# Performance work log

Measured on AMD Instinct MI355X. Metric: run time of the kernel, lower is better.

Reference implementation:

```python
import jax, jax.numpy as jnp
import numpy as np

B, S, D, NH = 4, 2048, 1024, 16
HD = D // NH  # head dim = 64

def setup_inputs() -> dict:
    key = jax.random.key(0)
    ks = jax.random.split(key, 10)
    sc = 0.02
    return {
        "hidden_states": jax.random.normal(ks[0], (B, S, D), jnp.float32),
        "attention_mask": jnp.ones((B, S), jnp.float32),
        "Wq": jax.random.normal(ks[1], (D, D), jnp.float32) * sc,
        "bq": jnp.zeros((D,), jnp.float32),
        "Wk": jax.random.normal(ks[2], (D, D), jnp.float32) * sc,
        "bk": jnp.zeros((D,), jnp.float32),
        "Wv": jax.random.normal(ks[3], (D, D), jnp.float32) * sc,
        "bv": jnp.zeros((D,), jnp.float32),
        "Wo": jax.random.normal(ks[4], (D, D), jnp.float32) * sc,
        "bo": jnp.zeros((D,), jnp.float32),
    }

def reference(hidden_states, attention_mask, Wq, bq, Wk, bk, Wv, bv, Wo, bo):
    # projections: torch Linear computes x @ W.T + b
    q = hidden_states @ Wq.T + bq
    k = hidden_states @ Wk.T + bk
    v = hidden_states @ Wv.T + bv
    # [B,S,D] -> [B,NH,S,HD]
    def split_heads(x):
        return x.reshape(B, S, NH, HD).transpose(0, 2, 1, 3)
    q, k, v = split_heads(q), split_heads(k), split_heads(v)
    scores = jnp.einsum('bhqd,bhkd->bhqk', q, k) / jnp.sqrt(jnp.float32(HD))
    ext_mask = (1.0 - attention_mask)[:, None, None, :] * -10000.0
    scores = scores + ext_mask
    probs = jax.nn.softmax(scores, axis=-1)
    ctx = jnp.einsum('bhqk,bhkd->bhqd', probs, v)
    ctx = ctx.transpose(0, 2, 1, 3).reshape(B, S, D)
    return ctx @ Wo.T + bo
```

## Files before the change

kernel.cpp:

```cpp
#include <hip/hip_runtime.h>

typedef __attribute__((ext_vector_type(8))) short bf16x8;
typedef __attribute__((ext_vector_type(4))) float f32x4;
typedef __attribute__((ext_vector_type(2))) unsigned u32x2;
typedef __attribute__((ext_vector_type(4))) unsigned u32x4;

#define NBATCH 4
#define NSEQ   2048
#define NDIM   1024
#define NHEAD  16
#define HDIM   64

static __device__ __forceinline__ unsigned short f2bf(float f) {
  unsigned u = __float_as_uint(f);
  u += 0x7fffu + ((u >> 16) & 1u);
  return (unsigned short)(u >> 16);
}

static __device__ __forceinline__ unsigned cvt_pk_bf16(float lo, float hi) {
  unsigned d;
  asm("v_cvt_pk_bf16_f32 %0, %1, %2" : "=v"(d) : "v"(lo), "v"(hi));
  return d;
}

static __device__ __forceinline__ void gload16(const void* g, void* l) {
  __builtin_amdgcn_global_load_lds(
      (const __attribute__((address_space(1))) unsigned*)g,
      (__attribute__((address_space(3))) unsigned*)l, 16, 0, 0);
}

__global__ __launch_bounds__(256) void cvt_kernel(
    const float* __restrict__ hs, const float* __restrict__ wq,
    const float* __restrict__ wk, const float* __restrict__ wv,
    const float* __restrict__ wo,
    unsigned short* __restrict__ hsb, unsigned short* __restrict__ wqb,
    unsigned short* __restrict__ wkb, unsigned short* __restrict__ wvb,
    unsigned short* __restrict__ wob) {
  long long t = (long long)blockIdx.x * blockDim.x + threadIdx.x;
  long long i4 = t * 4;
  const float* src; unsigned short* dst; long long base;
  if (i4 < 8388608LL) { src = hs; dst = hsb; base = i4; }
  else {
    long long j = i4 - 8388608LL;
    int w = (int)(j >> 20);
    base = j & 1048575LL;
    switch (w) { case 0: src=wq; dst=wqb; break; case 1: src=wk; dst=wkb; break;
                 case 2: src=wv; dst=wvb; break; default: src=wo; dst=wob; break; }
  }
  float4 v = *(const float4*)(src + base);
  unsigned short r0=f2bf(v.x), r1=f2bf(v.y), r2=f2bf(v.z), r3=f2bf(v.w);
  *(uint2*)(dst + base) = make_uint2((unsigned)r0 | ((unsigned)r1<<16),
                                     (unsigned)r2 | ((unsigned)r3<<16));
}

static __device__ __forceinline__ void gemm128(
    const unsigned short* __restrict__ A, const unsigned short* __restrict__ W,
    unsigned short* As, unsigned short* Bs, int m0, int n0, f32x4 (&acc)[4][4]) {
  const int tid = threadIdx.x;
  const int w = tid >> 6, l = tid & 63, g = l >> 4, r = l & 15;
  const int wm = w >> 1, wn = w & 1;
  const f32x4 z4 = {0.f, 0.f, 0.f, 0.f};
  #pragma unroll
  for (int i = 0; i < 4; ++i)
    #pragma unroll
    for (int j = 0; j < 4; ++j) acc[i][j] = z4;
  const int srow = (l >> 2);
  const int scol = (l & 3) * 8;
  for (int kt = 0; kt < 32; ++kt) {
    const int k0 = kt * 32;
    __syncthreads();
    #pragma unroll
    for (int i = 0; i < 2; ++i) {
      int c8 = w * 2 + i;
      int row = c8 * 16 + srow;
      gload16(A + (size_t)(m0 + row) * 1024 + k0 + scol, As + c8 * 512);
      gload16(W + (size_t)(n0 + row) * 1024 + k0 + scol, Bs + c8 * 512);
    }
    asm volatile("s_waitcnt vmcnt(0)" ::: "memory");
    __syncthreads();
    bf16x8 af[4], bf[4];
    #pragma unroll
    for (int ma = 0; ma < 4; ++ma)
      af[ma] = *(const bf16x8*)(As + (wm*64 + ma*16 + r) * 32 + g * 8);
    #pragma unroll
    for (int nb = 0; nb < 4; ++nb)
      bf[nb] = *(const bf16x8*)(Bs + (wn*64 + nb*16 + r) * 32 + g * 8);
    #pragma unroll
    for (int ma = 0; ma < 4; ++ma)
      #pragma unroll
      for (int nb = 0; nb < 4; ++nb)
        acc[ma][nb] = __builtin_amdgcn_mfma_f32_16x16x32_bf16(
            af[ma], bf[nb], acc[ma][nb], 0, 0, 0);
  }
}

__global__ __launch_bounds__(256) void qkv_gemm(
    const unsigned short* __restrict__ hsb,
    const unsigned short* __restrict__ wqb, const unsigned short* __restrict__ wkb,
    const unsigned short* __restrict__ wvb,
    const float* __restrict__ bq, const float* __restrict__ bk,
    const float* __restrict__ bv,
    unsigned short* __restrict__ qb, unsigned short* __restrict__ kb,
    unsigned short* __restrict__ vtb) {
  __shared__ unsigned short As[128*32], Bs[128*32];
  const int z = blockIdx.z;
  const unsigned short* W = (z == 0) ? wqb : (z == 1) ? wkb : wvb;
  const float* bias = (z == 0) ? bq : (z == 1) ? bk : bv;
  const int m0 = blockIdx.y * 128, n0 = blockIdx.x * 128;
  f32x4 acc[4][4];
  gemm128(hsb, W, As, Bs, m0, n0, acc);
  const int tid = threadIdx.x, w = tid >> 6, l = tid & 63, g = l >> 4, r = l & 15;
  const int wm = w >> 1, wn = w & 1;
  #pragma unroll
  for (int nb = 0; nb < 4; ++nb) {
    int n = n0 + wn*64 + nb*16 + r;
    float bval = bias[n];
    int h = n >> 6, d = n & 63;
    #pragma unroll
    for (int ma = 0; ma < 4; ++ma) {
      int mbase = m0 + wm*64 + ma*16 + g*4;
      if (z == 2) {
        int b = mbase >> 11, s0 = mbase & 2047;
        unsigned short u[4];
        #pragma unroll
        for (int j = 0; j < 4; ++j) u[j] = f2bf(acc[ma][nb][j] + bval);
        size_t idx = ((size_t)(b*16 + h) * 64 + d) * 2048 + s0;
        *(uint2*)(vtb + idx) = make_uint2((unsigned)u[0] | ((unsigned)u[1]<<16),
                                          (unsigned)u[2] | ((unsigned)u[3]<<16));
      } else {
        unsigned short* dst = (z == 0) ? qb : kb;
        float sc = (z == 0) ? 0.125f : 1.0f;
        #pragma unroll
        for (int j = 0; j < 4; ++j) {
          int m = mbase + j;
          int b = m >> 11, s = m & 2047;
          dst[((size_t)(b*16 + h) * 2048 + s) * 64 + d] = f2bf((acc[ma][nb][j] + bval) * sc);
        }
      }
    }
  }
}

__global__ __launch_bounds__(256) void flash_attn(
    const unsigned short* __restrict__ qg, const unsigned short* __restrict__ kg,
    const unsigned short* __restrict__ vg, const float* __restrict__ mask,
    unsigned short* __restrict__ ctxb) {
  __shared__ unsigned short Kl[2][4096], Vl[2][4096];
  const int tid = threadIdx.x, w = tid >> 6, l = tid & 63, g = l >> 4, r = l & 15;
  const int bh = blockIdx.y, b = bh >> 4, h = bh & 15;
  const unsigned short* qh = qg + (size_t)bh * 2048 * 64;
  const unsigned short* kh = kg + (size_t)bh * 2048 * 64;
  const unsigned short* vh = vg + (size_t)bh * 64 * 2048;
  const int q0 = blockIdx.x * 128;
  const int wq0 = q0 + w * 32;
  const float L2E = 1.44269504f;
  const float MC  = 14426.950408f;

  bf16x8 aq[2][2];
  #pragma unroll
  for (int mq = 0; mq < 2; ++mq)
    #pragma unroll
    for (int ks = 0; ks < 2; ++ks)
      aq[mq][ks] = *(const bf16x8*)(qh + (size_t)(wq0 + mq*16 + r) * 64 + ks*32 + g*8);

  const f32x4 z4 = {0.f, 0.f, 0.f, 0.f};
  f32x4 c[2][4];
  f32x4 cl[2];
  #pragma unroll
  for (int mq = 0; mq < 2; ++mq) {
    #pragma unroll
    for (int fn = 0; fn < 4; ++fn) c[mq][fn] = z4;
    cl[mq] = z4;
  }
  bf16x8 ones;
  #pragma unroll
  for (int i = 0; i < 8; ++i) ones[i] = (short)0x3F80;

  const int strow = l >> 3;
  const int stsl  = l & 7;

  #pragma unroll
  for (int i = 0; i < 2; ++i) {
    int c8 = w * 2 + i;
    int row = c8 * 8 + strow;
    int sl = stsl ^ (row & 7);
    gload16(kh + (size_t)row * 64 + sl * 8, &Kl[0][c8 * 512]);
    gload16(vh + (size_t)row * 2048 + sl * 8, &Vl[0][c8 * 512]);
  }
  asm volatile("s_waitcnt vmcnt(0)" ::: "memory");
  __syncthreads();

  for (int kt = 0; kt < 32; ++kt) {
    const int cur = kt & 1;
    const int k0 = kt * 64;
    const unsigned short* Kc = Kl[cur];
    const unsigned short* Vc = Vl[cur];

    if (kt < 31) {
      unsigned short* Kn = Kl[cur ^ 1];
      unsigned short* Vn = Vl[cur ^ 1];
      #pragma unroll
      for (int i = 0; i < 2; ++i) {
        int c8 = w * 2 + i;
        int row = c8 * 8 + strow;
        int sl = stsl ^ (row & 7);
        gload16(kh + (size_t)(k0 + 64 + row) * 64 + sl * 8, Kn + c8 * 512);
        gload16(vh + (size_t)row * 2048 + k0 + 64 + sl * 8, Vn + c8 * 512);
      }
    }

    float md[16];
    #pragma unroll
    for (int kq = 0; kq < 4; ++kq) {
      float4 m4 = *(const float4*)(mask + b * 2048 + k0 + kq*16 + g*4);
      md[kq*4+0] = fmaf(m4.x, MC, -MC);
      md[kq*4+1] = fmaf(m4.y, MC, -MC);
      md[kq*4+2] = fmaf(m4.z, MC, -MC);
      md[kq*4+3] = fmaf(m4.w, MC, -MC);
    }

    f32x4 sa[2][4];
    #pragma unroll
    for (int mq = 0; mq < 2; ++mq)
      #pragma unroll
      for (int kq = 0; kq < 4; ++kq) sa[mq][kq] = z4;
    #pragma unroll
    for (int kq = 0; kq < 4; ++kq) {
      int key = kq*16 + r;
      #pragma unroll
      for (int ks = 0; ks < 2; ++ks) {
        bf16x8 kf = *(const bf16x8*)(Kc + key*64 + (((ks*4 + g) ^ (key & 7)) * 8));
        sa[0][kq] = __builtin_amdgcn_mfma_f32_16x16x32_bf16(kf, aq[0][ks], sa[0][kq], 0,0,0);
        sa[1][kq] = __builtin_amdgcn_mfma_f32_16x16x32_bf16(kf, aq[1][ks], sa[1][kq], 0,0,0);
      }
    }

    bf16x8 pb[2][2];
    #pragma unroll
    for (int mq = 0; mq < 2; ++mq) {
      unsigned pk[4][2];
      #pragma unroll
      for (int kq = 0; kq < 4; ++kq) {
        float p0 = exp2f(fmaf(sa[mq][kq][0], L2E, md[kq*4+0]));
        float p1 = exp2f(fmaf(sa[mq][kq][1], L2E, md[kq*4+1]));
        float p2 = exp2f(fmaf(sa[mq][kq][2], L2E, md[kq*4+2]));
        float p3 = exp2f(fmaf(sa[mq][kq][3], L2E, md[kq*4+3]));
        pk[kq][0] = cvt_pk_bf16(p0, p1);
        pk[kq][1] = cvt_pk_bf16(p2, p3);
      }
      #pragma unroll
      for (int ch = 0; ch < 2; ++ch) {
        u32x4 fr;
        #pragma unroll
        for (int i = 0; i < 2; ++i) {
          u32x2 s1 = __builtin_amdgcn_permlane32_swap(pk[ch*2][i], pk[ch*2+1][i], false, false);
          u32x2 s2 = __builtin_amdgcn_permlane16_swap(s1.x, s1.y, false, false);
          fr[i]     = s2.x;
          fr[2 + i] = s2.y;
        }
        pb[mq][ch] = __builtin_bit_cast(bf16x8, fr);
      }
    }

    #pragma unroll
    for (int ks = 0; ks < 2; ++ks) {
      #pragma unroll
      for (int fn = 0; fn < 4; ++fn) {
        int vrow = fn*16 + r;
        bf16x8 vf = *(const bf16x8*)(Vc + vrow*64 + (((ks*4 + g) ^ (vrow & 7)) * 8));
        c[0][fn] = __builtin_amdgcn_mfma_f32_16x16x32_bf16(vf, pb[0][ks], c[0][fn], 0,0,0);
        c[1][fn] = __builtin_amdgcn_mfma_f32_16x16x32_bf16(vf, pb[1][ks], c[1][fn], 0,0,0);
      }
      cl[0] = __builtin_amdgcn_mfma_f32_16x16x32_bf16(ones, pb[0][ks], cl[0], 0,0,0);
      cl[1] = __builtin_amdgcn_mfma_f32_16x16x32_bf16(ones, pb[1][ks], cl[1], 0,0,0);
    }

    asm volatile("s_waitcnt vmcnt(0)" ::: "memory");
    __syncthreads();
  }

  #pragma unroll
  for (int mq = 0; mq < 2; ++mq) {
    float inv = 1.0f / cl[mq][0];
    int srow = q0 + w*32 + mq*16 + r;
    size_t base = ((size_t)(b * 2048 + srow)) * 1024 + h * 64;
    #pragma unroll
    for (int fn = 0; fn < 4; ++fn) {
      unsigned short u0 = f2bf(c[mq][fn][0] * inv);
      unsigned short u1 = f2bf(c[mq][fn][1] * inv);
      unsigned short u2 = f2bf(c[mq][fn][2] * inv);
      unsigned short u3 = f2bf(c[mq][fn][3] * inv);
      *(uint2*)(ctxb + base + fn*16 + g*4) =
          make_uint2((unsigned)u0 | ((unsigned)u1<<16),
                     (unsigned)u2 | ((unsigned)u3<<16));
    }
  }
}

__global__ __launch_bounds__(256) void out_gemm(
    const unsigned short* __restrict__ ctxb, const unsigned short* __restrict__ wob,
    const float* __restrict__ bo, float* __restrict__ out) {
  __shared__ unsigned short As[128*32], Bs[128*32];
  const int m0 = blockIdx.y * 128, n0 = blockIdx.x * 128;
  f32x4 acc[4][4];
  gemm128(ctxb, wob, As, Bs, m0, n0, acc);
  const int tid = threadIdx.x, w = tid >> 6, l = tid & 63, g = l >> 4, r = l & 15;
  const int wm = w >> 1, wn = w & 1;
  #pragma unroll
  for (int nb = 0; nb < 4; ++nb) {
    int n = n0 + wn*64 + nb*16 + r;
    float bval = bo[n];
    #pragma unroll
    for (int ma = 0; ma < 4; ++ma)
      #pragma unroll
      for (int j = 0; j < 4; ++j) {
        int m = m0 + wm*64 + ma*16 + g*4 + j;
        out[(size_t)m * 1024 + n] = acc[ma][nb][j] + bval;
      }
  }
}

extern "C" void kernel_launch(void* const* d_in, const int* in_sizes, int n_in,
                              void* d_out, int out_size, void* d_ws, size_t ws_size,
                              hipStream_t stream) {
  const float* hs   = (const float*)d_in[0];
  const float* mask = (const float*)d_in[1];
  const float* wq   = (const float*)d_in[2];
  const float* bq   = (const float*)d_in[3];
  const float* wk   = (const float*)d_in[4];
  const float* bk   = (const float*)d_in[5];
  const float* wv   = (const float*)d_in[6];
  const float* bv   = (const float*)d_in[7];
  const float* wo   = (const float*)d_in[8];
  const float* bo   = (const float*)d_in[9];
  float* out = (float*)d_out;
  char* ws = (char*)d_ws;
  unsigned short* hsb = (unsigned short*)(ws);
  unsigned short* wqb = (unsigned short*)(ws + (16ull << 20));
  unsigned short* wkb = (unsigned short*)(ws + (18ull << 20));
  unsigned short* wvb = (unsigned short*)(ws + (20ull << 20));
  unsigned short* wob = (unsigned short*)(ws + (22ull << 20));
  unsigned short* qb  = (unsigned short*)(ws + (24ull << 20));
  unsigned short* kb  = (unsigned short*)(ws + (40ull << 20));
  unsigned short* vtb = (unsigned short*)(ws + (56ull << 20));
  unsigned short* ctb = (unsigned short*)(ws + (72ull << 20));

  cvt_kernel<<<12288, 256, 0, stream>>>(hs, wq, wk, wv, wo, hsb, wqb, wkb, wvb, wob);
  qkv_gemm<<<dim3(8, 64, 3), 256, 0, stream>>>(hsb, wqb, wkb, wvb, bq, bk, bv, qb, kb, vtb);
  flash_attn<<<dim3(16, 64), 256, 0, stream>>>(qb, kb, vtb, mask, ctb);
  out_gemm<<<dim3(8, 64), 256, 0, stream>>>(ctb, wob, bo, out);
}
```

Baseline: 350.7 us.

## Load K/V fragments directly from global into registers, dropping LDS staging

The flash attention kernel no longer stages K and V tiles through double-buffered shared memory with per-tile barriers. Each wave now loads its K fragments straight from global memory into registers, prefetching the next tile's K during the current tile, and loads V fragments just before the PV MFMAs. It also raises wave priority around the MFMA blocks. This removes LDS traffic and block-wide syncs, but each of the four waves now fetches the same K/V data separately through the caches, and there is less latency hiding for the V loads.

```diff
diff --git a/kernel.cpp b/kernel.cpp
--- a/kernel.cpp
+++ b/kernel.cpp
@@ -145,17 +145,20 @@
     const unsigned short* __restrict__ qg, const unsigned short* __restrict__ kg,
     const unsigned short* __restrict__ vg, const float* __restrict__ mask,
     unsigned short* __restrict__ ctxb) {
-  __shared__ unsigned short Kl[2][4096], Vl[2][4096];
   const int tid = threadIdx.x, w = tid >> 6, l = tid & 63, g = l >> 4, r = l & 15;
   const int bh = blockIdx.y, b = bh >> 4, h = bh & 15;
   const unsigned short* qh = qg + (size_t)bh * 2048 * 64;
   const unsigned short* kh = kg + (size_t)bh * 2048 * 64;
   const unsigned short* vh = vg + (size_t)bh * 64 * 2048;
+  const float* maskb = mask + b * 2048;
   const int q0 = blockIdx.x * 128;
   const int wq0 = q0 + w * 32;
   const float L2E = 1.44269504f;
   const float MC  = 14426.950408f;
 
+  const unsigned short* kp = kh + (size_t)r * 64 + g * 8;
+  const unsigned short* vp = vh + (size_t)r * 2048 + g * 8;
+
   bf16x8 aq[2][2];
   #pragma unroll
   for (int mq = 0; mq < 2; ++mq)
@@ -176,63 +179,54 @@
   #pragma unroll
   for (int i = 0; i < 8; ++i) ones[i] = (short)0x3F80;
 
-  const int strow = l >> 3;
-  const int stsl  = l & 7;
-
-  #pragma unroll
-  for (int i = 0; i < 2; ++i) {
-    int c8 = w * 2 + i;
-    int row = c8 * 8 + strow;
-    int sl = stsl ^ (row & 7);
-    gload16(kh + (size_t)row * 64 + sl * 8, &Kl[0][c8 * 512]);
-    gload16(vh + (size_t)row * 2048 + sl * 8, &Vl[0][c8 * 512]);
-  }
-  asm volatile("s_waitcnt vmcnt(0)" ::: "memory");
-  __syncthreads();
-
-  for (int kt = 0; kt < 32; ++kt) {
-    const int cur = kt & 1;
-    const int k0 = kt * 64;
-    const unsigned short* Kc = Kl[cur];
-    const unsigned short* Vc = Vl[cur];
-
-    if (kt < 31) {
-      unsigned short* Kn = Kl[cur ^ 1];
-      unsigned short* Vn = Vl[cur ^ 1];
-      #pragma unroll
-      for (int i = 0; i < 2; ++i) {
-        int c8 = w * 2 + i;
-        int row = c8 * 8 + strow;
-        int sl = stsl ^ (row & 7);
-        gload16(kh + (size_t)(k0 + 64 + row) * 64 + sl * 8, Kn + c8 * 512);
-        gload16(vh + (size_t)row * 2048 + k0 + 64 + sl * 8, Vn + c8 * 512);
-      }
+  bf16x8 kf[4][2];
+  #pragma unroll
+  for (int kq = 0; kq < 4; ++kq)
+    #pragma unroll
+    for (int ks = 0; ks < 2; ++ks)
+      kf[kq][ks] = *(const bf16x8*)(kp + kq*1024 + ks*32);
+
+  for (int t = 0; t < 32; ++t) {
+    const int k0 = t * 64;
+
+    f32x4 sa[2][4];
+    #pragma unroll
+    for (int mq = 0; mq < 2; ++mq)
+      #pragma unroll
+      for (int kq = 0; kq < 4; ++kq) sa[mq][kq] = z4;
+    __builtin_amdgcn_s_setprio(1);
+    #pragma unroll
+    for (int kq = 0; kq < 4; ++kq)
+      #pragma unroll
+      for (int ks = 0; ks < 2; ++ks) {
+        sa[0][kq] = __builtin_amdgcn_mfma_f32_16x16x32_bf16(kf[kq][ks], aq[0][ks], sa[0][kq], 0,0,0);
+        sa[1][kq] = __builtin_amdgcn_mfma_f32_16x16x32_bf16(kf[kq][ks], aq[1][ks], sa[1][kq], 0,0,0);
+      }
+    __builtin_amdgcn_s_setprio(0);
+
+    bf16x8 vf[4][2];
+    #pragma unroll
+    for (int fn = 0; fn < 4; ++fn)
+      #pragma unroll
+      for (int ks = 0; ks < 2; ++ks)
+        vf[fn][ks] = *(const bf16x8*)(vp + fn*32768 + k0 + ks*32);
+
+    if (t < 31) {
+      #pragma unroll
+      for (int kq = 0; kq < 4; ++kq)
+        #pragma unroll
+        for (int ks = 0; ks < 2; ++ks)
+          kf[kq][ks] = *(const bf16x8*)(kp + (t+1)*4096 + kq*1024 + ks*32);
     }
 
     float md[16];
     #pragma unroll
     for (int kq = 0; kq < 4; ++kq) {
-      float4 m4 = *(const float4*)(mask + b * 2048 + k0 + kq*16 + g*4);
+      float4 m4 = *(const float4*)(maskb + k0 + kq*16 + g*4);
       md[kq*4+0] = fmaf(m4.x, MC, -MC);
       md[kq*4+1] = fmaf(m4.y, MC, -MC);
       md[kq*4+2] = fmaf(m4.z, MC, -MC);
       md[kq*4+3] = fmaf(m4.w, MC, -MC);
-    }
-
-    f32x4 sa[2][4];
-    #pragma unroll
-    for (int mq = 0; mq < 2; ++mq)
-      #pragma unroll
-      for (int kq = 0; kq < 4; ++kq) sa[mq][kq] = z4;
-    #pragma unroll
-    for (int kq = 0; kq < 4; ++kq) {
-      int key = kq*16 + r;
-      #pragma unroll
-      for (int ks = 0; ks < 2; ++ks) {
-        bf16x8 kf = *(const bf16x8*)(Kc + key*64 + (((ks*4 + g) ^ (key & 7)) * 8));
-        sa[0][kq] = __builtin_amdgcn_mfma_f32_16x16x32_bf16(kf, aq[0][ks], sa[0][kq], 0,0,0);
-        sa[1][kq] = __builtin_amdgcn_mfma_f32_16x16x32_bf16(kf, aq[1][ks], sa[1][kq], 0,0,0);
-      }
     }
 
     bf16x8 pb[2][2];
@@ -262,21 +256,18 @@
       }
     }
 
+    __builtin_amdgcn_s_setprio(1);
     #pragma unroll
     for (int ks = 0; ks < 2; ++ks) {
       #pragma unroll
       for (int fn = 0; fn < 4; ++fn) {
-        int vrow = fn*16 + r;
-        bf16x8 vf = *(const bf16x8*)(Vc + vrow*64 + (((ks*4 + g) ^ (vrow & 7)) * 8));
-        c[0][fn] = __builtin_amdgcn_mfma_f32_16x16x32_bf16(vf, pb[0][ks], c[0][fn], 0,0,0);
-        c[1][fn] = __builtin_amdgcn_mfma_f32_16x16x32_bf16(vf, pb[1][ks], c[1][fn], 0,0,0);
+        c[0][fn] = __builtin_amdgcn_mfma_f32_16x16x32_bf16(vf[fn][ks], pb[0][ks], c[0][fn], 0,0,0);
+        c[1][fn] = __builtin_amdgcn_mfma_f32_16x16x32_bf16(vf[fn][ks], pb[1][ks], c[1][fn], 0,0,0);
       }
       cl[0] = __builtin_amdgcn_mfma_f32_16x16x32_bf16(ones, pb[0][ks], cl[0], 0,0,0);
       cl[1] = __builtin_amdgcn_mfma_f32_16x16x32_bf16(ones, pb[1][ks], cl[1], 0,0,0);
     }
-
-    asm volatile("s_waitcnt vmcnt(0)" ::: "memory");
-    __syncthreads();
+    __builtin_amdgcn_s_setprio(0);
   }
 
   #pragma unroll
```

After: 458.9 us. 30.8% more time.
